# Optimization experiments

Hardware: AMD Instinct MI355X
Metric: run time of the kernel (lower is better)

## Reference

```python
import jax, jax.numpy as jnp
import numpy as np
from jax import lax

NAG = 3          # hardcoded in the torch module (query slices, catted_torches)
B = 4096         # batch_size per agent
H = 128          # hidden_dim
HEADS = 8
AD = H // HEADS  # attend_dim
STATE, ACT, SCAN = 48, 2, 256
OUTF, HID = 10, 256
NFEAT = 32 * (SCAN - 6)  # conv output features (two VALID convs: k5 then k3)
EPS = 1e-5

def leaky(x):
    return jnp.where(x >= 0, x, 0.01 * x)

def setup_inputs() -> dict:
    key = jax.random.key(0)
    ks = iter(jax.random.split(key, 40))
    def rn(shape, scale=0.05):
        return jax.random.normal(next(ks), shape, dtype=jnp.float32) * scale
    return {
        'obs':  jax.random.normal(next(ks), (NAG * B, STATE), jnp.float32),
        'acts': jax.random.normal(next(ks), (NAG * B, ACT), jnp.float32),
        'scan': jax.random.normal(next(ks), (NAG * B, SCAN), jnp.float32),
        'conv_w1': rn((32, 1, 5)),  'conv_b1': jnp.zeros((32,), jnp.float32),
        'conv_w2': rn((32, 32, 3)), 'conv_b2': jnp.zeros((32,), jnp.float32),
        'fc_w1': rn((256, NFEAT), 0.01), 'fc_b1': jnp.zeros((256,), jnp.float32),
        'fc_w2': rn((OUTF, 256)),        'fc_b2': jnp.zeros((OUTF,), jnp.float32),
        'enc_w': rn((H, STATE + ACT + OUTF)), 'enc_b': jnp.zeros((H,), jnp.float32),
        'Wk': rn((HEADS, AD, H)),
        'Wv': rn((HEADS, AD, H)), 'bv': jnp.zeros((HEADS, AD), jnp.float32),
        'Wq': rn((NAG, HEADS, AD, H)),
        'q1_w1': rn((HID, 2 * H)), 'q1_b1': jnp.zeros((HID,), jnp.float32),
        'q1_w2': rn((HID, HID)),   'q1_b2': jnp.zeros((HID,), jnp.float32),
        'q1_w3': rn((1, HID)),     'q1_b3': jnp.zeros((1,), jnp.float32),
        'q2_w1': rn((HID, 2 * H)), 'q2_b1': jnp.zeros((HID,), jnp.float32),
        'q2_w2': rn((HID, HID)),   'q2_b2': jnp.zeros((HID,), jnp.float32),
        'q2_w3': rn((1, HID)),     'q2_b3': jnp.zeros((1,), jnp.float32),
    }

def reference(obs, acts, scan, conv_w1, conv_b1, conv_w2, conv_b2,
              fc_w1, fc_b1, fc_w2, fc_b2, enc_w, enc_b, Wk, Wv, bv, Wq,
              q1_w1, q1_b1, q1_w2, q1_b2, q1_w3, q1_b3,
              q2_w1, q2_b1, q2_w2, q2_b2, q2_w3, q2_b3):
    dn = ('NCH', 'OIH', 'NCH')
    x = scan[:, None, :]                                            # [N,1,L]
    x = lax.conv_general_dilated(x, conv_w1, (1,), 'VALID', dimension_numbers=dn)
    x = jax.nn.relu(x + conv_b1[None, :, None])
    x = lax.conv_general_dilated(x, conv_w2, (1,), 'VALID', dimension_numbers=dn)
    x = jax.nn.relu(x + conv_b2[None, :, None])
    x = x.reshape(x.shape[0], -1)                                   # [N, NFEAT]
    x = jax.nn.relu(x @ fc_w1.T + fc_b1)
    feats = x @ fc_w2.T + fc_b2                                     # [N, OUTF]

    inps = jnp.concatenate([obs, acts, feats], axis=1)
    mu, var = inps.mean(0), inps.var(0)                             # BatchNorm1d (train, no affine)
    normed = (inps - mu) / jnp.sqrt(var + EPS)
    sa = leaky(normed @ enc_w.T + enc_b).reshape(NAG, B, H)         # [ag,B,H]

    keys = jnp.einsum('gbh,ndh->ngbd', sa, Wk)                      # [hd,ag,B,ad]
    vals = leaky(jnp.einsum('gbh,ndh->ngbd', sa, Wv) + bv[:, None, None, :])
    q = jnp.einsum('gbh,gndh->gnbd', sa, Wq)                        # [ag,hd,B,ad]

    logits = jnp.einsum('gnbd,nobd->gnbo', q, keys) / np.sqrt(AD)   # [ag,hd,B,ag]
    self_mask = jnp.eye(NAG, dtype=bool)[:, None, None, :]          # exclude own agent
    logits = jnp.where(self_mask, -jnp.inf, logits)
    w = jax.nn.softmax(logits, axis=-1)
    other = jnp.einsum('gnbo,nobd->gnbd', w, vals)                  # [ag,hd,B,ad]
    other = other.transpose(0, 2, 1, 3).reshape(NAG, B, H)          # heads concatenated

    emb = jnp.concatenate([sa, other], axis=2).reshape(NAG * B, 2 * H)

    def mlp(x, w1, b1, w2, b2, w3, b3):
        x = jax.nn.relu(x @ w1.T + b1)
        x = jax.nn.relu(x @ w2.T + b2)
        return x @ w3.T + b3

    q1 = mlp(emb, q1_w1, q1_b1, q1_w2, q1_b2, q1_w3, q1_b3)
    q2 = mlp(emb, q2_w1, q2_b1, q2_w2, q2_b2, q2_w3, q2_b3)
    return (q1, q2)
```

## Files before the change

kernel.cpp:

```cpp
#include <hip/hip_runtime.h>
#include <hip/hip_bf16.h>
#include <cstdint>
#include <cstddef>

typedef unsigned short u16;
typedef __attribute__((ext_vector_type(8))) __bf16 bf16x8;
typedef __attribute__((ext_vector_type(4))) float f32x4;

__device__ __forceinline__ u16 f2b(float f) {
  __hip_bfloat16 h = __float2bfloat16(f);
  return *reinterpret_cast<u16*>(&h);
}
__device__ __forceinline__ uint32_t pk2(float a, float b) {
  __hip_bfloat162 h = __float22bfloat162_rn(make_float2(a, b));
  return *reinterpret_cast<uint32_t*>(&h);
}
__device__ __forceinline__ float b2f(u16 u) {
  union { float f; uint32_t i; } x; x.i = ((uint32_t)u) << 16; return x.f;
}
__device__ __forceinline__ f32x4 mfma16(bf16x8 a, bf16x8 b, f32x4 c) {
  return __builtin_amdgcn_mfma_f32_16x16x32_bf16(a, b, c, 0, 0, 0);
}
__device__ __forceinline__ void async16(const void* g, void* l) {
  __builtin_amdgcn_global_load_lds((const __attribute__((address_space(1))) uint32_t*)g,
                                   (__attribute__((address_space(3))) uint32_t*)l, 16, 0, 0);
}

__global__ __launch_bounds__(256) void w1_perm(const float* __restrict__ w,
                                               u16* __restrict__ o) {
  __shared__ float L[8000];
  int j = blockIdx.x, tid = threadIdx.x;
  for (int i = tid; i < 8000; i += 256) L[i] = w[(size_t)j * 8000 + i];
  __syncthreads();
  for (int i = tid; i < 8000; i += 256) {
    int tt = i >> 5, c2 = i & 31;
    o[(size_t)j * 8000 + i] = f2b(L[c2 * 250 + tt]);
  }
}

struct CvtArgs {
  const float* src[13];
  void* dst[13];
  int cum[14];
  int kind[13];
};
__global__ __launch_bounds__(256) void f2b_multi(CvtArgs a, float* stats) {
  int i = blockIdx.x * 256 + threadIdx.x;
  if (blockIdx.x == 0 && threadIdx.x < 128) stats[threadIdx.x] = 0.f;
  int seg = 0;
  #pragma unroll
  for (int s = 1; s < 13; ++s) if (i >= a.cum[s]) seg = s;
  if (i < a.cum[13]) {
    int off = i - a.cum[seg];
    int kind = a.kind[seg];
    const float* src = a.src[seg];
    if (kind == 0) {
      ((u16*)a.dst[seg])[off] = f2b(src[off]);
    } else if (kind == 1) {
      int c2 = off / 96, rem = off - c2 * 96, kk = rem >> 5, c1 = rem & 31;
      ((u16*)a.dst[seg])[off] = f2b(src[(c2 * 32 + c1) * 3 + kk]);
    } else if (kind == 2) {
      int c1 = off >> 5, k = off & 31;
      ((u16*)a.dst[seg])[off] = f2b(k < 5 ? src[c1 * 5 + k] : 0.f);
    } else {
      ((float*)a.dst[seg])[off] = src[off];
    }
  }
}

__global__ __launch_bounds__(256) void conv_fused(
    const float* __restrict__ scan, const u16* __restrict__ w1g,
    const float* __restrict__ cb1, const u16* __restrict__ w2g,
    const float* __restrict__ cb2, u16* __restrict__ x) {
  __shared__ __align__(16) u16 A1[4][80 * 8];
  __shared__ __align__(16) u16 zb[4][8];
  __shared__ __align__(16) u16 h1[4][80 * 40];
  int tid = threadIdx.x, lane = tid & 63, wv = tid >> 6;
  int l15 = lane & 15, quad = lane >> 4;
  bf16x8 w1f[2];
  w1f[0] = *(const bf16x8*)&w1g[l15 * 32 + quad * 8];
  w1f[1] = *(const bf16x8*)&w1g[(16 + l15) * 32 + quad * 8];
  bf16x8 w2f[2][3];
  #pragma unroll
  for (int i = 0; i < 2; ++i)
    #pragma unroll
    for (int kk = 0; kk < 3; ++kk)
      w2f[i][kk] = *(const bf16x8*)&w2g[(i * 16 + l15) * 96 + kk * 32 + quad * 8];
  float cb1v[2][4], cb2v[2][4];
  #pragma unroll
  for (int i = 0; i < 2; ++i)
    #pragma unroll
    for (int r = 0; r < 4; ++r) {
      cb1v[i][r] = cb1[i * 16 + quad * 4 + r];
      cb2v[i][r] = cb2[i * 16 + quad * 4 + r];
    }
  if (lane < 8) zb[wv][lane] = 0;
  u16* A1w = &A1[wv][0];
  u16* h1w = &h1[wv][0];
  int p0 = wv * 64;
  f32x4 zero = {0.f, 0.f, 0.f, 0.f};
  #pragma unroll 1
  for (int rr = 0; rr < 4; ++rr) {
    int row = blockIdx.x * 4 + rr;
    const float* srow = scan + (size_t)row * 256;
    asm volatile("s_waitcnt lgkmcnt(0)" ::: "memory");
    {
      union { bf16x8 v; u16 u[8]; } pk_;
      int gp = p0 + lane;
      #pragma unroll
      for (int k = 0; k < 5; ++k) {
        int p = gp + k;
        pk_.u[k] = f2b(p < 256 ? srow[p] : 0.f);
      }
      pk_.u[5] = 0; pk_.u[6] = 0; pk_.u[7] = 0;
      *(bf16x8*)&A1w[lane * 8] = pk_.v;
      if (lane < 16) {
        union { bf16x8 v; u16 u[8]; } pq_;
        gp = p0 + 64 + lane;
        #pragma unroll
        for (int k = 0; k < 5; ++k) {
          int p = gp + k;
          pq_.u[k] = f2b(p < 256 ? srow[p] : 0.f);
        }
        pq_.u[5] = 0; pq_.u[6] = 0; pq_.u[7] = 0;
        *(bf16x8*)&A1w[(64 + lane) * 8] = pq_.v;
      }
    }
    asm volatile("s_waitcnt lgkmcnt(0)" ::: "memory");
    f32x4 acc1[5][2];
    #pragma unroll
    for (int nt = 0; nt < 5; ++nt) { acc1[nt][0] = zero; acc1[nt][1] = zero; }
    #pragma unroll
    for (int nt = 0; nt < 5; ++nt) {
      int lr = nt * 16 + l15;
      const u16* bp = (quad == 0) ? &A1w[lr * 8] : &zb[wv][0];
      bf16x8 bfr = *(const bf16x8*)bp;
      acc1[nt][0] = mfma16(w1f[0], bfr, acc1[nt][0]);
      acc1[nt][1] = mfma16(w1f[1], bfr, acc1[nt][1]);
    }
    #pragma unroll
    for (int nt = 0; nt < 5; ++nt) {
      int lr = nt * 16 + l15;
      #pragma unroll
      for (int mt = 0; mt < 2; ++mt) {
        float v0 = fmaxf(acc1[nt][mt][0] + cb1v[mt][0], 0.f);
        float v1 = fmaxf(acc1[nt][mt][1] + cb1v[mt][1], 0.f);
        float v2 = fmaxf(acc1[nt][mt][2] + cb1v[mt][2], 0.f);
        float v3 = fmaxf(acc1[nt][mt][3] + cb1v[mt][3], 0.f);
        uint2 u; u.x = pk2(v0, v1); u.y = pk2(v2, v3);
        *(uint2*)&h1w[lr * 40 + mt * 16 + quad * 4] = u;
      }
    }
    asm volatile("s_waitcnt lgkmcnt(0)" ::: "memory");
    f32x4 acc2[4][2];
    #pragma unroll
    for (int jj = 0; jj < 4; ++jj) { acc2[jj][0] = zero; acc2[jj][1] = zero; }
    #pragma unroll
    for (int kk = 0; kk < 3; ++kk) {
      #pragma unroll
      for (int jj = 0; jj < 4; ++jj) {
        int lt = jj * 16 + l15 + kk;
        bf16x8 h = *(const bf16x8*)&h1w[lt * 40 + quad * 8];
        acc2[jj][0] = mfma16(w2f[0][kk], h, acc2[jj][0]);
        acc2[jj][1] = mfma16(w2f[1][kk], h, acc2[jj][1]);
      }
    }
    u16* xr = x + (size_t)row * 8000;
    #pragma unroll
    for (int jj = 0; jj < 4; ++jj) {
      int t = p0 + jj * 16 + l15;
      if (t < 250) {
        #pragma unroll
        for (int i = 0; i < 2; ++i) {
          float v0 = fmaxf(acc2[jj][i][0] + cb2v[i][0], 0.f);
          float v1 = fmaxf(acc2[jj][i][1] + cb2v[i][1], 0.f);
          float v2 = fmaxf(acc2[jj][i][2] + cb2v[i][2], 0.f);
          float v3 = fmaxf(acc2[jj][i][3] + cb2v[i][3], 0.f);
          uint2 u; u.x = pk2(v0, v1); u.y = pk2(v2, v3);
          *(uint2*)&xr[t * 32 + i * 16 + quad * 4] = u;
        }
      }
    }
  }
}

template <int MODE, int MROWS>
__global__ __launch_bounds__(256) void gemm_bt(
    const u16* __restrict__ A, int lda, const u16* __restrict__ W, int ldw,
    const float* __restrict__ bias, float* __restrict__ outF,
    u16* __restrict__ outB, int ldo, int nst, int a_sel, size_t out_zoff) {
  constexpr int AI = (MROWS * 8) / 256;
  __shared__ __align__(16) u16 As[2][MROWS * 64];
  __shared__ __align__(16) u16 Bs[2][128 * 64];
  int tid = threadIdx.x;
  int m0 = blockIdx.y * MROWS;
  int sel = (MODE == 4) ? blockIdx.x : 0;
  int n0 = (MODE == 4) ? 0 : blockIdx.x * 128;
  if (MODE == 4) {
    size_t woff = (sel < 2) ? (size_t)sel * 128 : (size_t)(256 + (m0 >> 12) * 128);
    W += woff * 128;
    outB += (size_t)sel * 12288 * 128;
  }
  if (a_sel) A += (size_t)(blockIdx.x >> 1) * a_sel;
  int kbase = blockIdx.z * nst * 64;
  if (MODE == 0) outF += (size_t)blockIdx.z * out_zoff;
  const u16* Ap = A + (size_t)m0 * lda + kbase;
  const u16* Wp = W + (size_t)n0 * ldw + kbase;
  int lane = tid & 63, wv = tid >> 6;
  int l15 = lane & 15, quad = lane >> 4;
  int wm = (wv >> 1) * (MROWS / 2), wn = (wv & 1) * 64;
  constexpr int MI = MROWS / 32;
  f32x4 zero = {0.f, 0.f, 0.f, 0.f};
  f32x4 acc[MI][4];
  #pragma unroll
  for (int i = 0; i < MI; ++i)
    #pragma unroll
    for (int j = 0; j < 4; ++j) acc[i][j] = zero;

  int sraA[AI], sofA[AI], sdsA[AI];
  #pragma unroll
  for (int it = 0; it < AI; ++it) {
    int c = it * 256 + tid;
    int row = c >> 3, slot = c & 7;
    sraA[it] = row;
    sofA[it] = ((slot ^ (row & 7)) * 8);
    sdsA[it] = c * 8;
  }
  int sraW[4], sofW[4], sdsW[4];
  #pragma unroll
  for (int it = 0; it < 4; ++it) {
    int c = it * 256 + tid;
    int row = c >> 3, slot = c & 7;
    sraW[it] = row;
    sofW[it] = ((slot ^ (row & 7)) * 8);
    sdsW[it] = c * 8;
  }
  int rslot[2];
  rslot[0] = ((quad ^ (l15 & 7)) * 8);
  rslot[1] = (((4 + quad) ^ (l15 & 7)) * 8);

  #pragma unroll 1
  for (int st = 0; st < nst; ++st) {
    if (st == 0) {
      #pragma unroll
      for (int it = 0; it < AI; ++it)
        async16(Ap + (size_t)sraA[it] * lda + sofA[it], &As[0][sdsA[it]]);
      #pragma unroll
      for (int it = 0; it < 4; ++it)
        async16(Wp + (size_t)sraW[it] * ldw + sofW[it], &Bs[0][sdsW[it]]);
    }
    __syncthreads();
    if (st + 1 < nst) {
      const u16* An = Ap + (st + 1) * 64;
      const u16* Wn = Wp + (st + 1) * 64;
      u16* Ad = &As[(st + 1) & 1][0];
      u16* Bd = &Bs[(st + 1) & 1][0];
      #pragma unroll
      for (int it = 0; it < AI; ++it)
        async16(An + (size_t)sraA[it] * lda + sofA[it], Ad + sdsA[it]);
      #pragma unroll
      for (int it = 0; it < 4; ++it)
        async16(Wn + (size_t)sraW[it] * ldw + sofW[it], Bd + sdsW[it]);
    }
    const u16* Ab = &As[st & 1][0];
    const u16* Bb = &Bs[st & 1][0];
    #pragma unroll
    for (int s = 0; s < 2; ++s) {
      bf16x8 af[MI], bfr[4];
      #pragma unroll
      for (int i = 0; i < MI; ++i)
        af[i] = *(const bf16x8*)&Ab[(wm + i * 16 + l15) * 64 + rslot[s]];
      #pragma unroll
      for (int j = 0; j < 4; ++j)
        bfr[j] = *(const bf16x8*)&Bb[(wn + j * 16 + l15) * 64 + rslot[s]];
      #pragma unroll
      for (int i = 0; i < MI; ++i)
        #pragma unroll
        for (int j = 0; j < 4; ++j) acc[i][j] = mfma16(af[i], bfr[j], acc[i][j]);
    }
  }
  #pragma unroll
  for (int i = 0; i < MI; ++i) {
    int mb = m0 + wm + i * 16 + quad * 4;
    #pragma unroll
    for (int j = 0; j < 4; ++j) {
      int n = n0 + wn + j * 16 + l15;
      float bv_ = (MODE == 1 || MODE == 4) ? bias[n] : 0.f;
      #pragma unroll
      for (int r = 0; r < 4; ++r) {
        float v = acc[i][j][r];
        if (MODE == 0) {
          outF[(size_t)(mb + r) * ldo + n] = v;
        } else if (MODE == 1) {
          v = fmaxf(v + bv_, 0.f);
          outB[(size_t)(mb + r) * ldo + n] = f2b(v);
        } else {
          if (sel == 1) { v += bv_; v = v >= 0.f ? v : 0.01f * v; }
          outB[(size_t)(mb + r) * ldo + n] = f2b(v);
        }
      }
    }
  }
}

__global__ __launch_bounds__(256) void fc2_stats(
    const float* __restrict__ hparts, const float* __restrict__ b1,
    const float* __restrict__ w2, const float* __restrict__ b2,
    const float* __restrict__ obs, const float* __restrict__ acts,
    float* __restrict__ inps, float* __restrict__ stats) {
  __shared__ float hL[32 * 260];
  __shared__ float w2L[10 * 260];
  __shared__ float b1L[256];
  __shared__ float ipL[32 * 61];
  int tid = threadIdx.x, r0 = blockIdx.x * 32;
  b1L[tid] = b1[tid];
  for (int i = tid; i < 2560; i += 256) w2L[(i >> 8) * 260 + (i & 255)] = w2[i];
  for (int i = tid; i < 32 * 48; i += 256) {
    int r = i / 48, f = i - r * 48;
    ipL[r * 61 + f] = obs[(size_t)(r0 + r) * 48 + f];
  }
  if (tid < 64) {
    int r = tid >> 1, f = tid & 1;
    ipL[r * 61 + 48 + f] = acts[(size_t)(r0 + r) * 2 + f];
  }
  __syncthreads();
  const size_t HS = (size_t)12288 * 256;
  for (int i = tid; i < 32 * 256; i += 256) {
    int r = i >> 8, c = i & 255;
    size_t g = (size_t)(r0 + r) * 256 + c;
    float v = b1L[c] + hparts[g] + hparts[g + HS] + hparts[g + 2 * HS] +
              hparts[g + 3 * HS] + hparts[g + 4 * HS];
    hL[r * 260 + c] = fmaxf(v, 0.f);
  }
  __syncthreads();
  {
    int r = tid >> 3, ob = tid & 7;
    for (int o = ob; o < 10; o += 8) {
      float a = 0.f;
      #pragma unroll 8
      for (int c = 0; c < 256; ++c) a += hL[r * 260 + c] * w2L[o * 260 + c];
      ipL[r * 61 + 50 + o] = a + b2[o];
    }
  }
  __syncthreads();
  for (int i = tid; i < 32 * 60; i += 256) {
    int r = i / 60, f = i - r * 60;
    inps[(size_t)(r0 + r) * 64 + f] = ipL[r * 61 + f];
  }
  if (tid < 60) {
    float s = 0.f, s2 = 0.f;
    for (int r = 0; r < 32; ++r) {
      float v = ipL[r * 61 + tid];
      s += v; s2 += v * v;
    }
    atomicAdd(&stats[tid], s);
    atomicAdd(&stats[64 + tid], s2);
  }
}

__global__ __launch_bounds__(256) void enc_kernel(
    const float* __restrict__ inps, const float* __restrict__ stats,
    const float* __restrict__ enc_w, const float* __restrict__ enc_b,
    u16* __restrict__ sab) {
  __shared__ float ewL[128 * 61];
  __shared__ float nrm[32 * 61];
  __shared__ float ebL[128];
  __shared__ float muL[60], ivL[60];
  int tid = threadIdx.x, r0 = blockIdx.x * 32;
  if (tid < 128) ebL[tid] = enc_b[tid];
  if (tid < 60) {
    float s = stats[tid], s2 = stats[64 + tid];
    float mu = s * (1.f / 12288.f);
    float var = s2 * (1.f / 12288.f) - mu * mu;
    muL[tid] = mu;
    ivL[tid] = rsqrtf(var + 1e-5f);
  }
  for (int i = tid; i < 128 * 60; i += 256) {
    int h = i / 60, f = i - h * 60;
    ewL[h * 61 + f] = enc_w[i];
  }
  __syncthreads();
  for (int i = tid; i < 32 * 60; i += 256) {
    int r = i / 60, f = i - r * 60;
    nrm[r * 61 + f] = (inps[(size_t)(r0 + r) * 64 + f] - muL[f]) * ivL[f];
  }
  __syncthreads();
  for (int i = tid; i < 32 * 128; i += 256) {
    int r = i >> 7, h = i & 127;
    float a = ebL[h];
    #pragma unroll 4
    for (int f = 0; f < 60; ++f) a += nrm[r * 61 + f] * ewL[h * 61 + f];
    a = a >= 0.f ? a : 0.01f * a;
    sab[(size_t)(r0 + r) * 128 + h] = f2b(a);
  }
}

__global__ __launch_bounds__(128) void attn_combine(
    const u16* __restrict__ qb, const u16* __restrict__ keysb,
    const u16* __restrict__ valsb, const u16* __restrict__ sab,
    u16* __restrict__ emb) {
  __shared__ float qL[3][128], kL[3][128], vL[3][128];
  __shared__ float lg[3][8][3], wgt[3][8][3];
  int b = blockIdx.x, t = threadIdx.x;
  #pragma unroll
  for (int o = 0; o < 3; ++o) {
    size_t base = (size_t)(o * 4096 + b) * 128 + t;
    qL[o][t] = b2f(qb[base]);
    kL[o][t] = b2f(keysb[base]);
    vL[o][t] = b2f(valsb[base]);
  }
  __syncthreads();
  if (t < 72) {
    int g = t / 24, n = (t / 3) % 8, o = t % 3;
    float a = 0.f;
    #pragma unroll
    for (int d = 0; d < 16; ++d) a += qL[g][n * 16 + d] * kL[o][n * 16 + d];
    lg[g][n][o] = (o == g) ? -1e30f : a * 0.25f;
  }
  __syncthreads();
  if (t < 24) {
    int g = t / 8, n = t % 8;
    float m = fmaxf(fmaxf(lg[g][n][0], lg[g][n][1]), lg[g][n][2]);
    float e0 = expf(lg[g][n][0] - m), e1 = expf(lg[g][n][1] - m),
          e2 = expf(lg[g][n][2] - m);
    float inv = 1.f / (e0 + e1 + e2);
    wgt[g][n][0] = e0 * inv; wgt[g][n][1] = e1 * inv; wgt[g][n][2] = e2 * inv;
  }
  __syncthreads();
  int n = t >> 4, d = t & 15;
  #pragma unroll
  for (int g = 0; g < 3; ++g) {
    float o_ = wgt[g][n][0] * vL[0][n * 16 + d] +
               wgt[g][n][1] * vL[1][n * 16 + d] +
               wgt[g][n][2] * vL[2][n * 16 + d];
    size_t rbase = (size_t)(g * 4096 + b) * 256;
    emb[rbase + 128 + t] = f2b(o_);
    emb[rbase + t] = sab[(size_t)(g * 4096 + b) * 128 + t];
  }
}

__global__ __launch_bounds__(256) void final_dot(
    const u16* __restrict__ t2ab, const float* __restrict__ w3a,
    const float* __restrict__ b3a, const float* __restrict__ w3b,
    const float* __restrict__ b3b, float* __restrict__ out) {
  int wv = threadIdx.x >> 6, lane = threadIdx.x & 63;
  int row = blockIdx.x * 4 + wv;
  float sa_ = 0.f, sb_ = 0.f;
  #pragma unroll
  for (int e = 0; e < 4; ++e) {
    int c = lane * 4 + e;
    sa_ += b2f(t2ab[(size_t)row * 512 + c]) * w3a[c];
    sb_ += b2f(t2ab[(size_t)row * 512 + 256 + c]) * w3b[c];
  }
  #pragma unroll
  for (int off = 32; off; off >>= 1) {
    sa_ += __shfl_down(sa_, off);
    sb_ += __shfl_down(sb_, off);
  }
  if (lane == 0) {
    out[row] = sa_ + b3a[0];
    out[12288 + row] = sb_ + b3b[0];
  }
}

extern "C" void kernel_launch(void* const* d_in, const int* in_sizes, int n_in,
                              void* d_out, int out_size, void* d_ws,
                              size_t ws_size, hipStream_t stream) {
  const float* obs  = (const float*)d_in[0];
  const float* acts = (const float*)d_in[1];
  const float* scan = (const float*)d_in[2];
  const float* cw1  = (const float*)d_in[3];
  const float* cb1  = (const float*)d_in[4];
  const float* cw2  = (const float*)d_in[5];
  const float* cb2  = (const float*)d_in[6];
  const float* fw1  = (const float*)d_in[7];
  const float* fb1  = (const float*)d_in[8];
  const float* fw2  = (const float*)d_in[9];
  const float* fb2  = (const float*)d_in[10];
  const float* encw = (const float*)d_in[11];
  const float* encb = (const float*)d_in[12];
  const float* Wk   = (const float*)d_in[13];
  const float* Wv   = (const float*)d_in[14];
  const float* bv   = (const float*)d_in[15];
  const float* Wq   = (const float*)d_in[16];
  const float* q1w1 = (const float*)d_in[17];
  const float* q1b1 = (const float*)d_in[18];
  const float* q1w2 = (const float*)d_in[19];
  const float* q1b2 = (const float*)d_in[20];
  const float* q1w3 = (const float*)d_in[21];
  const float* q1b3 = (const float*)d_in[22];
  const float* q2w1 = (const float*)d_in[23];
  const float* q2b1 = (const float*)d_in[24];
  const float* q2w2 = (const float*)d_in[25];
  const float* q2b2 = (const float*)d_in[26];
  const float* q2w3 = (const float*)d_in[27];
  const float* q2b3 = (const float*)d_in[28];
  float* out = (float*)d_out;
  char* ws = (char*)d_ws;
  if (ws_size < 264400000u) return;

  u16*   x     = (u16*)(ws + 0);
  u16*   w1b   = (u16*)(ws + 196608000);
  float* hpart = (float*)(ws + 200704000);
  float* stats = (float*)(ws + 263618560);
  u16*   wkvqb = (u16*)(ws + 263619584);
  u16*   m1ab  = (u16*)(ws + 263783424);
  u16*   m2ab  = (u16*)(ws + 264045568);
  u16*   w2g   = (u16*)(ws + 264307712);
  u16*   w1g   = (u16*)(ws + 264313856);
  float* bc1   = (float*)(ws + 264315904);
  float* bc2   = (float*)(ws + 264317952);
  float* inps  = (float*)(ws + 0);
  u16*   sab   = (u16*)(ws + 3145728);
  u16*   kvqb  = (u16*)(ws + 6291456);
  u16*   embb  = (u16*)(ws + 15728640);
  u16*   t1ab  = (u16*)(ws + 22020096);
  u16*   t2ab  = (u16*)(ws + 34603008);
  u16*   keysb = kvqb;
  u16*   valsb = kvqb + (size_t)12288 * 128;
  u16*   qb    = kvqb + (size_t)2 * 12288 * 128;

  w1_perm<<<256, 256, 0, stream>>>(fw1, w1b);
  CvtArgs ca;
  const float* srcs[13] = {Wk, Wv, Wq, q1w1, q2w1, q1w2, q2w2, cw2, cw1,
                           q1b1, q2b1, q1b2, q2b2};
  void* dsts[13] = {wkvqb, wkvqb + 16384, wkvqb + 32768, m1ab, m1ab + 65536,
                    m2ab, m2ab + 65536, w2g, w1g, bc1, bc1 + 256, bc2, bc2 + 256};
  const int sz[13] = {16384, 16384, 49152, 65536, 65536, 65536, 65536,
                      3072, 1024, 256, 256, 256, 256};
  const int kinds[13] = {0, 0, 0, 0, 0, 0, 0, 1, 2, 3, 3, 3, 3};
  int cum = 0;
  ca.cum[0] = 0;
  for (int i = 0; i < 13; ++i) {
    ca.src[i] = srcs[i]; ca.dst[i] = dsts[i]; ca.kind[i] = kinds[i];
    cum += sz[i]; ca.cum[i + 1] = cum;
  }
  f2b_multi<<<(cum + 255) / 256, 256, 0, stream>>>(ca, stats);

  conv_fused<<<3072, 256, 0, stream>>>(scan, w1g, cb1, w2g, cb2, x);
  gemm_bt<0, 64><<<dim3(2, 192, 5), 256, 0, stream>>>(
      x, 8000, w1b, 8000, nullptr, hpart, nullptr, 256, 25, 0,
      (size_t)12288 * 256);
  fc2_stats<<<384, 256, 0, stream>>>(hpart, fb1, fw2, fb2, obs, acts, inps, stats);
  enc_kernel<<<384, 256, 0, stream>>>(inps, stats, encw, encb, sab);
  gemm_bt<4, 64><<<dim3(3, 192, 1), 256, 0, stream>>>(
      sab, 128, wkvqb, 128, bv, nullptr, kvqb, 128, 2, 0, 0);
  attn_combine<<<4096, 128, 0, stream>>>(qb, keysb, valsb, sab, embb);
  gemm_bt<1, 64><<<dim3(4, 192, 1), 256, 0, stream>>>(
      embb, 256, m1ab, 256, bc1, nullptr, t1ab, 512, 4, 0, 0);
  gemm_bt<1, 64><<<dim3(4, 192, 1), 256, 0, stream>>>(
      t1ab, 512, m2ab, 256, bc2, nullptr, t2ab, 512, 4, 256, 0);
  final_dot<<<3072, 256, 0, stream>>>(t2ab, q1w3, q1b3, q2w3, q2b3, out);
}
```

Measured before the change: 385.3 us.

## Restructure conv kernel to one row per block with permuted channel output

```diff
diff --git a/kernel.cpp b/kernel.cpp
--- a/kernel.cpp
+++ b/kernel.cpp
@@ -33,7 +33,8 @@
   for (int i = tid; i < 8000; i += 256) L[i] = w[(size_t)j * 8000 + i];
   __syncthreads();
   for (int i = tid; i < 8000; i += 256) {
-    int tt = i >> 5, c2 = i & 31;
+    int tt = i >> 5, cc = i & 31;
+    int c2 = ((cc >> 2) & 1) * 16 + (cc >> 3) * 4 + (cc & 3);
     o[(size_t)j * 8000 + i] = f2b(L[c2 * 250 + tt]);
   }
 }
@@ -72,11 +73,26 @@
     const float* __restrict__ scan, const u16* __restrict__ w1g,
     const float* __restrict__ cb1, const u16* __restrict__ w2g,
     const float* __restrict__ cb2, u16* __restrict__ x) {
-  __shared__ __align__(16) u16 A1[4][80 * 8];
-  __shared__ __align__(16) u16 zb[4][8];
-  __shared__ __align__(16) u16 h1[4][80 * 40];
+  __shared__ __align__(16) u16 A1[256 * 8];
+  __shared__ __align__(16) u16 zbuf[4 * 8];
+  __shared__ __align__(16) u16 h1T[258 * 40];
   int tid = threadIdx.x, lane = tid & 63, wv = tid >> 6;
   int l15 = lane & 15, quad = lane >> 4;
+  const float* srow = scan + (size_t)blockIdx.x * 256;
+  float sv[5];
+  #pragma unroll
+  for (int k = 0; k < 5; ++k) {
+    int p = tid + k;
+    sv[k] = (p < 256) ? srow[p] : 0.f;
+  }
+  union { bf16x8 v; uint32_t d[4]; } pk_;
+  pk_.d[0] = pk2(sv[0], sv[1]);
+  pk_.d[1] = pk2(sv[2], sv[3]);
+  pk_.d[2] = pk2(sv[4], 0.f);
+  pk_.d[3] = 0;
+  *(bf16x8*)&A1[tid * 8] = pk_.v;
+  if (lane < 8) zbuf[wv * 8 + lane] = 0;
+  if (tid < 80) h1T[256 * 40 + tid] = 0;
   bf16x8 w1f[2];
   w1f[0] = *(const bf16x8*)&w1g[l15 * 32 + quad * 8];
   w1f[1] = *(const bf16x8*)&w1g[(16 + l15) * 32 + quad * 8];
@@ -94,53 +110,23 @@
       cb1v[i][r] = cb1[i * 16 + quad * 4 + r];
       cb2v[i][r] = cb2[i * 16 + quad * 4 + r];
     }
-  if (lane < 8) zb[wv][lane] = 0;
-  u16* A1w = &A1[wv][0];
-  u16* h1w = &h1[wv][0];
-  int p0 = wv * 64;
+  asm volatile("s_waitcnt lgkmcnt(0)" ::: "memory");
   f32x4 zero = {0.f, 0.f, 0.f, 0.f};
-  #pragma unroll 1
-  for (int rr = 0; rr < 4; ++rr) {
-    int row = blockIdx.x * 4 + rr;
-    const float* srow = scan + (size_t)row * 256;
-    asm volatile("s_waitcnt lgkmcnt(0)" ::: "memory");
-    {
-      union { bf16x8 v; u16 u[8]; } pk_;
-      int gp = p0 + lane;
-      #pragma unroll
-      for (int k = 0; k < 5; ++k) {
-        int p = gp + k;
-        pk_.u[k] = f2b(p < 256 ? srow[p] : 0.f);
-      }
-      pk_.u[5] = 0; pk_.u[6] = 0; pk_.u[7] = 0;
-      *(bf16x8*)&A1w[lane * 8] = pk_.v;
-      if (lane < 16) {
-        union { bf16x8 v; u16 u[8]; } pq_;
-        gp = p0 + 64 + lane;
-        #pragma unroll
-        for (int k = 0; k < 5; ++k) {
-          int p = gp + k;
-          pq_.u[k] = f2b(p < 256 ? srow[p] : 0.f);
-        }
-        pq_.u[5] = 0; pq_.u[6] = 0; pq_.u[7] = 0;
-        *(bf16x8*)&A1w[(64 + lane) * 8] = pq_.v;
-      }
-    }
-    asm volatile("s_waitcnt lgkmcnt(0)" ::: "memory");
-    f32x4 acc1[5][2];
-    #pragma unroll
-    for (int nt = 0; nt < 5; ++nt) { acc1[nt][0] = zero; acc1[nt][1] = zero; }
-    #pragma unroll
-    for (int nt = 0; nt < 5; ++nt) {
-      int lr = nt * 16 + l15;
-      const u16* bp = (quad == 0) ? &A1w[lr * 8] : &zb[wv][0];
+  {
+    f32x4 acc1[4][2];
+    #pragma unroll
+    for (int nt = 0; nt < 4; ++nt) { acc1[nt][0] = zero; acc1[nt][1] = zero; }
+    #pragma unroll
+    for (int nt = 0; nt < 4; ++nt) {
+      int p = (wv * 4 + nt) * 16 + l15;
+      const u16* bp = (quad == 0) ? &A1[p * 8] : &zbuf[wv * 8];
       bf16x8 bfr = *(const bf16x8*)bp;
       acc1[nt][0] = mfma16(w1f[0], bfr, acc1[nt][0]);
       acc1[nt][1] = mfma16(w1f[1], bfr, acc1[nt][1]);
     }
     #pragma unroll
-    for (int nt = 0; nt < 5; ++nt) {
-      int lr = nt * 16 + l15;
+    for (int nt = 0; nt < 4; ++nt) {
+      int p = (wv * 4 + nt) * 16 + l15;
       #pragma unroll
       for (int mt = 0; mt < 2; ++mt) {
         float v0 = fmaxf(acc1[nt][mt][0] + cb1v[mt][0], 0.f);
@@ -148,38 +134,40 @@
         float v2 = fmaxf(acc1[nt][mt][2] + cb1v[mt][2], 0.f);
         float v3 = fmaxf(acc1[nt][mt][3] + cb1v[mt][3], 0.f);
         uint2 u; u.x = pk2(v0, v1); u.y = pk2(v2, v3);
-        *(uint2*)&h1w[lr * 40 + mt * 16 + quad * 4] = u;
+        *(uint2*)&h1T[p * 40 + mt * 16 + quad * 4] = u;
       }
     }
-    asm volatile("s_waitcnt lgkmcnt(0)" ::: "memory");
-    f32x4 acc2[4][2];
-    #pragma unroll
-    for (int jj = 0; jj < 4; ++jj) { acc2[jj][0] = zero; acc2[jj][1] = zero; }
-    #pragma unroll
-    for (int kk = 0; kk < 3; ++kk) {
-      #pragma unroll
-      for (int jj = 0; jj < 4; ++jj) {
-        int lt = jj * 16 + l15 + kk;
-        bf16x8 h = *(const bf16x8*)&h1w[lt * 40 + quad * 8];
-        acc2[jj][0] = mfma16(w2f[0][kk], h, acc2[jj][0]);
-        acc2[jj][1] = mfma16(w2f[1][kk], h, acc2[jj][1]);
+  }
+  __syncthreads();
+  f32x4 acc2[4][2];
+  #pragma unroll
+  for (int jj = 0; jj < 4; ++jj) { acc2[jj][0] = zero; acc2[jj][1] = zero; }
+  #pragma unroll
+  for (int kk = 0; kk < 3; ++kk) {
+    #pragma unroll
+    for (int jj = 0; jj < 4; ++jj) {
+      int t = (wv * 4 + jj) * 16 + l15 + kk;
+      bf16x8 h = *(const bf16x8*)&h1T[t * 40 + quad * 8];
+      acc2[jj][0] = mfma16(w2f[0][kk], h, acc2[jj][0]);
+      acc2[jj][1] = mfma16(w2f[1][kk], h, acc2[jj][1]);
+    }
+  }
+  u16* xr = x + (size_t)blockIdx.x * 8000;
+  #pragma unroll
+  for (int jj = 0; jj < 4; ++jj) {
+    int t = (wv * 4 + jj) * 16 + l15;
+    if (t < 250) {
+      union { bf16x8 v; uint32_t d[4]; } o_;
+      #pragma unroll
+      for (int i = 0; i < 2; ++i) {
+        float v0 = fmaxf(acc2[jj][i][0] + cb2v[i][0], 0.f);
+        float v1 = fmaxf(acc2[jj][i][1] + cb2v[i][1], 0.f);
+        float v2 = fmaxf(acc2[jj][i][2] + cb2v[i][2], 0.f);
+        float v3 = fmaxf(acc2[jj][i][3] + cb2v[i][3], 0.f);
+        o_.d[i * 2]     = pk2(v0, v1);
+        o_.d[i * 2 + 1] = pk2(v2, v3);
       }
-    }
-    u16* xr = x + (size_t)row * 8000;
-    #pragma unroll
-    for (int jj = 0; jj < 4; ++jj) {
-      int t = p0 + jj * 16 + l15;
-      if (t < 250) {
-        #pragma unroll
-        for (int i = 0; i < 2; ++i) {
-          float v0 = fmaxf(acc2[jj][i][0] + cb2v[i][0], 0.f);
-          float v1 = fmaxf(acc2[jj][i][1] + cb2v[i][1], 0.f);
-          float v2 = fmaxf(acc2[jj][i][2] + cb2v[i][2], 0.f);
-          float v3 = fmaxf(acc2[jj][i][3] + cb2v[i][3], 0.f);
-          uint2 u; u.x = pk2(v0, v1); u.y = pk2(v2, v3);
-          *(uint2*)&xr[t * 32 + i * 16 + quad * 4] = u;
-        }
-      }
+      *(bf16x8*)&xr[t * 32 + quad * 8] = o_.v;
     }
   }
 }
@@ -537,7 +525,7 @@
   }
   f2b_multi<<<(cum + 255) / 256, 256, 0, stream>>>(ca, stats);
 
-  conv_fused<<<3072, 256, 0, stream>>>(scan, w1g, cb1, w2g, cb2, x);
+  conv_fused<<<12288, 256, 0, stream>>>(scan, w1g, cb1, w2g, cb2, x);
   gemm_bt<0, 64><<<dim3(2, 192, 5), 256, 0, stream>>>(
       x, 8000, w1b, 8000, nullptr, hpart, nullptr, 256, 25, 0,
       (size_t)12288 * 256);
```

Result: faster. 364.3 us (-5.5%).
